# Kernel tuning notes

Measured on AMD Instinct MI355X. Metric: run time of the kernel, lower is better.

The kernel has to match this reference:

```python
import jax, jax.numpy as jnp
import numpy as np

N, E, CIN, H, HEADS, B = 50000, 800000, 16, 64, 3, 64
D0 = HEADS * H            # conv1 out (heads concatenated) = 192
D1 = D0 + CIN             # x1 dim = 208
D2 = 2 * D1               # x2 dim = 416
MLP_IN = 3 * D2           # 1248
MLP_HID = MLP_IN // 2     # 624
EPS = 1e-5


def setup_inputs() -> dict:
    key = jax.random.key(0)
    ks = jax.random.split(key, 24)
    r = lambda k, s, sc=0.05: (jax.random.normal(k, s, dtype=jnp.float32) * sc)
    inp = {
        'x': jax.random.normal(ks[0], (N, CIN), dtype=jnp.float32),
        'edge_index': jax.random.randint(ks[1], (2, E), 0, N, dtype=jnp.int32),
        'edge_attr': jax.random.normal(ks[2], (E, 4), dtype=jnp.float32),
        'batch': jnp.sort(jax.random.randint(ks[3], (N,), 0, B, dtype=jnp.int32)),
        # conv1 (GeneralConv, heads=3, concat): msg/edge/self linears -> D0
        'W_msg1': r(ks[4], (CIN, D0)), 'b_msg1': jnp.zeros((D0,), jnp.float32),
        'W_edge1': r(ks[5], (4, D0)), 'b_edge1': jnp.zeros((D0,), jnp.float32),
        'W_self1': r(ks[6], (CIN, D0)), 'b_self1': jnp.zeros((D0,), jnp.float32),
        'g1': jnp.ones((D0,), jnp.float32), 'be1': jnp.zeros((D0,), jnp.float32),
        # conv2 (GeneralConv, heads=1, in==out -> identity self)
        'W_msg2': r(ks[7], (D1, D1)), 'b_msg2': jnp.zeros((D1,), jnp.float32),
        'W_edge2': r(ks[8], (4, D1)), 'b_edge2': jnp.zeros((D1,), jnp.float32),
        'g2': jnp.ones((D1,), jnp.float32), 'be2': jnp.zeros((D1,), jnp.float32),
        # MLP head
        'W_l1': r(ks[9], (MLP_IN, MLP_HID)), 'b_l1': jnp.zeros((MLP_HID,), jnp.float32),
        'alpha': jnp.asarray(0.25, jnp.float32),  # PReLU default
        'W_l2': r(ks[10], (MLP_HID, 2)), 'b_l2': jnp.zeros((2,), jnp.float32),
    }
    return inp


def _bn(h, g, b):
    m = h.mean(axis=0)
    v = h.var(axis=0)  # biased, like torch BatchNorm training mode
    return (h - m) * jax.lax.rsqrt(v + EPS) * g + b


def reference(x, edge_index, edge_attr, batch,
              W_msg1, b_msg1, W_edge1, b_edge1, W_self1, b_self1, g1, be1,
              W_msg2, b_msg2, W_edge2, b_edge2, g2, be2,
              W_l1, b_l1, alpha, W_l2, b_l2):
    src, dst = edge_index[0], edge_index[1]
    # conv1: gather -> linear msg + edge feature -> scatter-add -> + self linear
    m1 = x[src] @ W_msg1 + b_msg1 + edge_attr @ W_edge1 + b_edge1   # [E, D0]
    h1 = jax.ops.segment_sum(m1, dst, num_segments=N) + (x @ W_self1 + b_self1)
    h1 = _bn(h1, g1, be1)
    x1 = jnp.concatenate([h1, x], axis=1)                           # [N, D1]
    # conv2 (identity self-connection since in==out)
    m2 = x1[src] @ W_msg2 + b_msg2 + edge_attr @ W_edge2 + b_edge2  # [E, D1]
    h2 = jax.ops.segment_sum(m2, dst, num_segments=N) + x1
    h2 = _bn(h2, g2, be2)
    x2 = jnp.concatenate([h2, x1], axis=1)                          # [N, D2]
    # global add / mean / max pooling by graph id
    s = jax.ops.segment_sum(x2, batch, num_segments=B)
    cnt = jax.ops.segment_sum(jnp.ones((x2.shape[0], 1), x2.dtype), batch, num_segments=B)
    mean = s / jnp.maximum(cnt, 1.0)
    mx = jax.ops.segment_max(x2, batch, num_segments=B)
    pooled = jnp.concatenate([s, mx, mean], axis=1)                 # [B, 3*D2]
    # MLP head: Linear -> Dropout(0) -> PReLU -> Linear -> log_softmax
    h = pooled @ W_l1 + b_l1
    h = jnp.where(h >= 0, h, alpha * h)
    logits = h @ W_l2 + b_l2
    return jax.nn.log_softmax(logits, axis=-1)
```

## Files before the change

### kernel.cpp

```cpp
#include <hip/hip_runtime.h>

typedef __attribute__((ext_vector_type(8))) short short8;
typedef __attribute__((ext_vector_type(4))) float f32x4;
typedef unsigned short u16;
typedef unsigned int u32;

__device__ __forceinline__ u16 f2bf(float f) {
  u32 u = __float_as_uint(f);
  u = (u + 0x7fffu + ((u >> 16) & 1u)) >> 16;
  return (u16)u;
}
__device__ __forceinline__ float bf2f(u16 v) { return __uint_as_float((u32)v << 16); }
__device__ __forceinline__ void atomAddF(float* p, float v) { unsafeAtomicAdd(p, v); }
__device__ __forceinline__ void addp(float* v, u32 p) {
  v[0] += bf2f((u16)p);
  v[1] += bf2f((u16)(p >> 16));
}

__global__ void prep_k(const float* __restrict__ Wm1, const float* __restrict__ We1,
                       const float* __restrict__ Ws1, const float* __restrict__ Wm2,
                       const float* __restrict__ Wl1, const float* __restrict__ x,
                       const int* __restrict__ batch, u16* __restrict__ Wp1,
                       u16* __restrict__ Wp2, u16* __restrict__ Wp3,
                       u16* __restrict__ xbf, int* __restrict__ gstart,
                       int* __restrict__ gend, int* __restrict__ deg,
                       float* __restrict__ bns1p, float* __restrict__ bns2p, int N, int E) {
  int tid = blockIdx.x * 256 + threadIdx.x;
  if (tid < 64 * 192) {
    int k = tid / 192, n = tid % 192;
    float v = 0.f;
    if (k < 16) v = Wm1[k * 192 + n];
    else if (k < 20) v = We1[(k - 16) * 192 + n];
    else if (k < 36) v = Ws1[(k - 20) * 192 + n];
    Wp1[((k >> 3) * 192 + n) * 8 + (k & 7)] = f2bf(v);
  }
  if (tid < 224 * 208) {
    int k = tid / 208, n = tid % 208;
    float v = (k < 208) ? Wm2[k * 208 + n] : 0.f;
    Wp2[((k >> 3) * 208 + n) * 8 + (k & 7)] = f2bf(v);
  }
  if (tid < N * 8) {
    float2 p = *(const float2*)(x + (size_t)tid * 2);
    *(u32*)(xbf + (size_t)tid * 2) = (u32)f2bf(p.x) | ((u32)f2bf(p.y) << 16);
  }
  if (tid < N) {
    int b = batch[tid];
    if (tid == 0 || batch[tid - 1] != b) gstart[b] = tid;
    if (tid == N - 1 || batch[tid + 1] != b) gend[b] = tid;
    deg[tid] = 0;
  }
  if (tid < 64 * 384) bns1p[tid] = 0.f;
  if (tid < 64 * 832) bns2p[tid] = 0.f;
  if (tid < 1248 * 624) {
    int k = tid / 624, n = tid % 624;
    Wp3[((size_t)(k >> 3) * 624 + n) * 8 + (k & 7)] = f2bf(Wl1[(size_t)k * 624 + n]);
  }
}

__global__ void count_k(const int* __restrict__ ei, int* __restrict__ deg,
                        int* __restrict__ ord, int E) {
  int e = blockIdx.x * 256 + threadIdx.x;
  if (e >= E) return;
  ord[e] = atomicAdd(&deg[ei[E + e]], 1);
}

__global__ void scanA_k(const int* __restrict__ deg, int* __restrict__ bsum, int N) {
  __shared__ int sh[256];
  int t = threadIdx.x;
  int i = blockIdx.x * 256 + t;
  sh[t] = (i < N) ? deg[i] : 0;
  __syncthreads();
  for (int off = 128; off > 0; off >>= 1) {
    if (t < off) sh[t] += sh[t + off];
    __syncthreads();
  }
  if (t == 0) bsum[blockIdx.x] = sh[0];
}

__global__ void scanC_k(const int* __restrict__ deg, const int* __restrict__ bsum,
                        int* __restrict__ rowptr, int N, int nb) {
  __shared__ int sb2[256];
  __shared__ int sh[256];
  int t = threadIdx.x;
  int bv = (t < nb) ? bsum[t] : 0;
  sb2[t] = bv;
  __syncthreads();
  for (int off = 1; off < 256; off <<= 1) {
    int u = (t >= off) ? sb2[t - off] : 0;
    __syncthreads();
    sb2[t] += u;
    __syncthreads();
  }
  int bpref = (blockIdx.x == 0) ? 0 : sb2[blockIdx.x - 1];
  int i = blockIdx.x * 256 + t;
  int d = (i < N) ? deg[i] : 0;
  sh[t] = d;
  __syncthreads();
  for (int off = 1; off < 256; off <<= 1) {
    int u = (t >= off) ? sh[t - off] : 0;
    __syncthreads();
    sh[t] += u;
    __syncthreads();
  }
  int excl = sh[t] - d + bpref;
  if (i < N) {
    rowptr[i] = excl;
    if (i == N - 1) rowptr[N] = excl + d;
  }
}

__global__ void scatter_k(const int* __restrict__ ei, const float* __restrict__ ea,
                          const int* __restrict__ ord, const int* __restrict__ rowptr,
                          int4* __restrict__ se16, int E) {
  int e = blockIdx.x * 256 + threadIdx.x;
  if (e >= E) return;
  int s = ei[e], d = ei[E + e];
  float4 w = *(const float4*)(ea + (size_t)e * 4);
  int slot = rowptr[d] + ord[e];
  int4 ent;
  ent.x = s;
  ent.y = (int)((u32)f2bf(w.x) | ((u32)f2bf(w.y) << 16));
  ent.z = (int)((u32)f2bf(w.z) | ((u32)f2bf(w.w) << 16));
  ent.w = 0;
  se16[slot] = ent;
}

__global__ void __launch_bounds__(512) conv1_k(
    const int4* __restrict__ se16, const int* __restrict__ rowptr,
    const u16* __restrict__ xbf, const u16* __restrict__ Bp,
    const float* __restrict__ bm1, const float* __restrict__ be1,
    const float* __restrict__ bs1, u16* __restrict__ acc1c, u16* __restrict__ h1bf,
    float* __restrict__ bns1p, int N) {
  __shared__ __align__(16) u16 Uls[32][72];
  __shared__ float degls[32];
  int tid = threadIdx.x;
  int nl = tid >> 4, q = tid & 15;
  int n = blockIdx.x * 32 + nl;
  bool nval = n < N;
  int j0 = nval ? rowptr[n] : 0;
  int j1 = nval ? rowptr[n + 1] : 0;
  float v[20];
#pragma unroll
  for (int i = 0; i < 20; ++i) v[i] = 0.f;
  {
    int j = j0 + q;
    bool a0 = j < j1, a1 = (j + 16) < j1;
    int jj0 = a0 ? j : 0;
    int jj1 = a1 ? (j + 16) : 0;
    int4 p0 = se16[jj0];
    int4 p1 = se16[jj1];
    const uint4* xs0 = (const uint4*)(xbf + (size_t)(a0 ? p0.x : 0) * 16);
    uint4 x00 = xs0[0], x01 = xs0[1];
    const uint4* xs1 = (const uint4*)(xbf + (size_t)(a1 ? p1.x : 0) * 16);
    uint4 x10 = xs1[0], x11 = xs1[1];
    if (a0) {
      addp(v + 0, x00.x); addp(v + 2, x00.y); addp(v + 4, x00.z); addp(v + 6, x00.w);
      addp(v + 8, x01.x); addp(v + 10, x01.y); addp(v + 12, x01.z); addp(v + 14, x01.w);
      addp(v + 16, (u32)p0.y); addp(v + 18, (u32)p0.z);
    }
    if (a1) {
      addp(v + 0, x10.x); addp(v + 2, x10.y); addp(v + 4, x10.z); addp(v + 6, x10.w);
      addp(v + 8, x11.x); addp(v + 10, x11.y); addp(v + 12, x11.z); addp(v + 14, x11.w);
      addp(v + 16, (u32)p1.y); addp(v + 18, (u32)p1.z);
    }
    for (j += 32; j < j1; j += 16) {
      int4 p = se16[j];
      const uint4* xs = (const uint4*)(xbf + (size_t)p.x * 16);
      uint4 x0 = xs[0], x1 = xs[1];
      addp(v + 0, x0.x); addp(v + 2, x0.y); addp(v + 4, x0.z); addp(v + 6, x0.w);
      addp(v + 8, x1.x); addp(v + 10, x1.y); addp(v + 12, x1.z); addp(v + 14, x1.w);
      addp(v + 16, (u32)p.y); addp(v + 18, (u32)p.z);
    }
  }
#pragma unroll
  for (int i = 0; i < 20; ++i) {
    v[i] += __shfl_xor(v[i], 1);
    v[i] += __shfl_xor(v[i], 2);
    v[i] += __shfl_xor(v[i], 4);
    v[i] += __shfl_xor(v[i], 8);
  }
  float degf = (float)(j1 - j0);
  const u16* xr = xbf + (size_t)n * 16;
  {
    u32 w2[2];
#pragma unroll
    for (int jj = 0; jj < 2; ++jj) {
      int t0 = q * 4 + 2 * jj, t1 = t0 + 1;
      u16 b0 = (t0 < 20) ? f2bf(v[t0]) : ((t0 < 36 && nval) ? xr[t0 - 20] : (u16)0);
      u16 b1 = (t1 < 20) ? f2bf(v[t1]) : ((t1 < 36 && nval) ? xr[t1 - 20] : (u16)0);
      w2[jj] = (u32)b0 | ((u32)b1 << 16);
    }
    *(uint2*)&Uls[nl][q * 4] = make_uint2(w2[0], w2[1]);
  }
  if (nval) {
    int t0 = q * 2, t1 = t0 + 1;
    float f0 = (t0 < 20) ? v[t0] : ((t0 == 20) ? degf : 0.f);
    float f1 = (t1 < 20) ? v[t1] : ((t1 == 20) ? degf : 0.f);
    *(u32*)(acc1c + (size_t)n * 32 + q * 2) = (u32)f2bf(f0) | ((u32)f2bf(f1) << 16);
  }
  if (q == 0) degls[nl] = degf;
  __syncthreads();
  int w = tid >> 6, lane = tid & 63, rc = lane & 15, qd = lane >> 4;
  int slice = (blockIdx.x & 63) * 384;
  for (int job = w; job < 24; job += 8) {
    int mt = job / 12, nt = job % 12;
    f32x4 acc = {0.f, 0.f, 0.f, 0.f};
#pragma unroll
    for (int kb = 0; kb < 2; ++kb) {
      short8 av = *(const short8*)&Uls[mt * 16 + rc][kb * 32 + qd * 8];
      short8 bv = *(const short8*)(Bp + (size_t)((kb * 4 + qd) * 192 + nt * 16 + rc) * 8);
      acc = __builtin_amdgcn_mfma_f32_16x16x32_bf16(av, bv, acc, 0, 0, 0);
    }
    int col = nt * 16 + rc;
    float bb = bm1[col] + be1[col], bsv = bs1[col];
    float ps = 0.f, pq = 0.f;
#pragma unroll
    for (int r = 0; r < 4; ++r) {
      int ml = mt * 16 + qd * 4 + r;
      int m = blockIdx.x * 32 + ml;
      float val = acc[r] + degls[ml] * bb + bsv;
      if (m < N) {
        h1bf[(size_t)m * 192 + col] = f2bf(val);
        ps += val;
        pq += val * val;
      }
    }
    ps += __shfl_xor(ps, 16); ps += __shfl_xor(ps, 32);
    pq += __shfl_xor(pq, 16); pq += __shfl_xor(pq, 32);
    if (qd == 0) {
      atomAddF(&bns1p[slice + col], ps);
      atomAddF(&bns1p[slice + 192 + col], pq);
    }
  }
}

__global__ void bnfin1_k(const float* __restrict__ bns1p, const float* __restrict__ g1,
                         const float* __restrict__ bta1, float Ninv,
                         float* __restrict__ aff1) {
  int c = threadIdx.x;
  if (c >= 192) return;
  float sm = 0.f, sq = 0.f;
  for (int k = 0; k < 64; ++k) {
    sm += bns1p[k * 384 + c];
    sq += bns1p[k * 384 + 192 + c];
  }
  float m1 = sm * Ninv;
  float var = sq * Ninv - m1 * m1;
  float s1 = g1[c] * rsqrtf(var + 1e-5f);
  aff1[c] = s1;
  aff1[192 + c] = bta1[c] - m1 * s1;
}

__global__ void __launch_bounds__(512) conv2_k(
    const int4* __restrict__ se16, const int* __restrict__ rowptr,
    const u16* __restrict__ acc1c, const u16* __restrict__ h1bf,
    const u16* __restrict__ xbf, const u16* __restrict__ Bp1, const u16* __restrict__ Bp2,
    const float* __restrict__ bm1, const float* __restrict__ be1,
    const float* __restrict__ bs1, const float* __restrict__ aff1,
    const float* __restrict__ We2, const float* __restrict__ bm2,
    const float* __restrict__ be2, float* __restrict__ bns2p,
    u16* __restrict__ h2bf, int N) {
  __shared__ __align__(16) u16 Uls[32][72];
  __shared__ __align__(16) u16 Vls[32][232];
  __shared__ __align__(16) u16 X1ls[32][208];
  __shared__ float degls[32], sdegls[32], eals[32][4];
  int tid = threadIdx.x;
  int nl = tid >> 4, q = tid & 15;
  int n = blockIdx.x * 32 + nl;
  bool nval = n < N;
  int j0 = nval ? rowptr[n] : 0;
  int j1 = nval ? rowptr[n + 1] : 0;
  int base = blockIdx.x * 32;

  uint4 sg0, sg1, sgx;
  int r0 = tid / 24, c0 = tid % 24;
  int r1 = (tid + 512) / 24, c1 = (tid + 512) % 24;
  {
    int gr = base + r0;
    sg0 = (gr < N) ? *(const uint4*)(h1bf + (size_t)gr * 192 + c0 * 8)
                   : make_uint4(0, 0, 0, 0);
  }
  if (tid < 256) {
    int gr = base + r1;
    sg1 = (gr < N) ? *(const uint4*)(h1bf + (size_t)gr * 192 + c1 * 8)
                   : make_uint4(0, 0, 0, 0);
  }
  if (tid < 64) {
    int gr = base + (tid >> 1);
    sgx = (gr < N) ? *(const uint4*)(xbf + (size_t)gr * 16 + (tid & 1) * 8)
                   : make_uint4(0, 0, 0, 0);
  }

  float v[21];
#pragma unroll
  for (int i = 0; i < 21; ++i) v[i] = 0.f;
  {
    int j = j0 + q;
    bool a0 = j < j1, a1 = (j + 16) < j1;
    int jj0 = a0 ? j : 0;
    int jj1 = a1 ? (j + 16) : 0;
    int4 p0 = se16[jj0];
    int4 p1 = se16[jj1];
    const uint4* cr0 = (const uint4*)(acc1c + (size_t)(a0 ? p0.x : 0) * 32);
    uint4 c00 = cr0[0], c01 = cr0[1], c02 = cr0[2];
    const uint4* cr1 = (const uint4*)(acc1c + (size_t)(a1 ? p1.x : 0) * 32);
    uint4 c10 = cr1[0], c11 = cr1[1], c12 = cr1[2];
    if (a0) {
      addp(v + 0, c00.x); addp(v + 2, c00.y); addp(v + 4, c00.z); addp(v + 6, c00.w);
      addp(v + 8, c01.x); addp(v + 10, c01.y); addp(v + 12, c01.z); addp(v + 14, c01.w);
      addp(v + 16, c02.x); addp(v + 18, c02.y);
      v[20] += bf2f((u16)c02.z);
    }
    if (a1) {
      addp(v + 0, c10.x); addp(v + 2, c10.y); addp(v + 4, c10.z); addp(v + 6, c10.w);
      addp(v + 8, c11.x); addp(v + 10, c11.y); addp(v + 12, c11.z); addp(v + 14, c11.w);
      addp(v + 16, c12.x); addp(v + 18, c12.y);
      v[20] += bf2f((u16)c12.z);
    }
    for (j += 32; j < j1; j += 16) {
      int s = se16[j].x;
      const uint4* cr = (const uint4*)(acc1c + (size_t)s * 32);
      uint4 c0 = cr[0], c1 = cr[1], c2 = cr[2];
      addp(v + 0, c0.x); addp(v + 2, c0.y); addp(v + 4, c0.z); addp(v + 6, c0.w);
      addp(v + 8, c1.x); addp(v + 10, c1.y); addp(v + 12, c1.z); addp(v + 14, c1.w);
      addp(v + 16, c2.x); addp(v + 18, c2.y);
      v[20] += bf2f((u16)c2.z);
    }
  }

  *(uint4*)&X1ls[r0][c0 * 8] = sg0;
  if (tid < 256) *(uint4*)&X1ls[r1][c1 * 8] = sg1;
  if (tid < 64) *(uint4*)&X1ls[tid >> 1][192 + (tid & 1) * 8] = sgx;

#pragma unroll
  for (int i = 0; i < 21; ++i) {
    v[i] += __shfl_xor(v[i], 1);
    v[i] += __shfl_xor(v[i], 2);
    v[i] += __shfl_xor(v[i], 4);
    v[i] += __shfl_xor(v[i], 8);
  }
  const u16* selfr = acc1c + (size_t)n * 32;
  {
    u32 w2[2];
#pragma unroll
    for (int jj = 0; jj < 2; ++jj) {
      int t0 = q * 4 + 2 * jj, t1 = t0 + 1;
      u16 b0 = (t0 < 20) ? f2bf(v[t0]) : ((t0 < 36 && nval) ? selfr[t0 - 20] : (u16)0);
      u16 b1 = (t1 < 20) ? f2bf(v[t1]) : ((t1 < 36 && nval) ? selfr[t1 - 20] : (u16)0);
      w2[jj] = (u32)b0 | ((u32)b1 << 16);
    }
    *(uint2*)&Uls[nl][q * 4] = make_uint2(w2[0], w2[1]);
  }
  {
    int t0 = q * 2, t1 = t0 + 1;
    u16 b0 = (t0 < 16 && nval) ? selfr[t0] : (u16)0;
    u16 b1 = (t1 < 16 && nval) ? selfr[t1] : (u16)0;
    *(u32*)&Vls[nl][192 + q * 2] = (u32)b0 | ((u32)b1 << 16);
  }
  if (q == 0) sdegls[nl] = v[20];
  if (q == 1) degls[nl] = nval ? bf2f(selfr[20]) : 0.f;
  if (q == 2) {
#pragma unroll
    for (int k = 0; k < 4; ++k) eals[nl][k] = nval ? bf2f(selfr[16 + k]) : 0.f;
  }
  __syncthreads();
  int w = tid >> 6, lane = tid & 63, rc = lane & 15, qd = lane >> 4;
  for (int job = w; job < 24; job += 8) {
    int mt = job / 12, nt = job % 12;
    f32x4 acc = {0.f, 0.f, 0.f, 0.f};
#pragma unroll
    for (int kb = 0; kb < 2; ++kb) {
      short8 av = *(const short8*)&Uls[mt * 16 + rc][kb * 32 + qd * 8];
      short8 bv = *(const short8*)(Bp1 + (size_t)((kb * 4 + qd) * 192 + nt * 16 + rc) * 8);
      acc = __builtin_amdgcn_mfma_f32_16x16x32_bf16(av, bv, acc, 0, 0, 0);
    }
    int col = nt * 16 + rc;
    float s1 = aff1[col], t1 = aff1[192 + col];
    float bb = bm1[col] + be1[col], bsv = bs1[col];
#pragma unroll
    for (int r = 0; r < 4; ++r) {
      int ml = mt * 16 + qd * 4 + r;
      float qv = acc[r] + sdegls[ml] * bb + degls[ml] * bsv;
      Vls[ml][col] = f2bf(qv * s1 + degls[ml] * t1);
    }
  }
  __syncthreads();
  int slice = (blockIdx.x & 63) * 832;
  for (int job = w; job < 26; job += 8) {
    int mt = job / 13, nt = job % 13;
    f32x4 acc = {0.f, 0.f, 0.f, 0.f};
#pragma unroll
    for (int kb = 0; kb < 7; ++kb) {
      short8 av = *(const short8*)&Vls[mt * 16 + rc][kb * 32 + qd * 8];
      short8 bv = *(const short8*)(Bp2 + (size_t)((kb * 4 + qd) * 208 + nt * 16 + rc) * 8);
      acc = __builtin_amdgcn_mfma_f32_16x16x32_bf16(av, bv, acc, 0, 0, 0);
    }
    int col = nt * 16 + rc;
    float w0 = We2[col], w1 = We2[208 + col], w2 = We2[416 + col], w3 = We2[624 + col];
    float bb2 = bm2[col] + be2[col];
    bool c192 = col < 192;
    float s1 = c192 ? aff1[col] : 0.f;
    float t1 = c192 ? aff1[192 + col] : 0.f;
    float ps = 0.f, pq = 0.f;
#pragma unroll
    for (int r = 0; r < 4; ++r) {
      int ml = mt * 16 + qd * 4 + r;
      int m = blockIdx.x * 32 + ml;
      bool mv = m < N;
      float x1 = bf2f(X1ls[ml][col]);
      if (c192) x1 = x1 * s1 + t1;
      float val = acc[r] + eals[ml][0] * w0 + eals[ml][1] * w1 + eals[ml][2] * w2 +
                  eals[ml][3] * w3 + degls[ml] * bb2 + x1;
      if (mv) {
        h2bf[(size_t)m * 208 + col] = f2bf(val);
        ps += val;
        pq += val * val;
      }
    }
    ps += __shfl_xor(ps, 16); ps += __shfl_xor(ps, 32);
    pq += __shfl_xor(pq, 16); pq += __shfl_xor(pq, 32);
    if (qd == 0) {
      atomAddF(&bns2p[slice + col], ps);
      atomAddF(&bns2p[slice + 416 + col], pq);
    }
  }
}

__global__ void bnfin2_k(const float* __restrict__ bns2p, const float* __restrict__ aff1,
                         const float* __restrict__ g2, const float* __restrict__ bta2,
                         float Ninv, float* __restrict__ aff) {
  int f = blockIdx.x * 256 + threadIdx.x;
  if (f >= 416) return;
  float sc, sh;
  if (f < 208) {
    float sm = 0.f, sq = 0.f;
    for (int k = 0; k < 64; ++k) {
      sm += bns2p[k * 832 + f];
      sq += bns2p[k * 832 + 416 + f];
    }
    float m2 = sm * Ninv;
    float var = sq * Ninv - m2 * m2;
    sc = g2[f] * rsqrtf(var + 1e-5f);
    sh = bta2[f] - m2 * sc;
  } else if (f < 400) {
    sc = aff1[f - 208];
    sh = aff1[192 + (f - 208)];
  } else {
    sc = 1.f;
    sh = 0.f;
  }
  aff[f] = sc;
  aff[416 + f] = sh;
}

__global__ void pool_k(const u16* __restrict__ h2bf, const u16* __restrict__ h1bf,
                       const u16* __restrict__ xbf, const float* __restrict__ aff,
                       const int* __restrict__ gstart, const int* __restrict__ gend,
                       float* __restrict__ psp, float* __restrict__ pmp) {
  int b = blockIdx.x, sub = blockIdx.y;
  int t = threadIdx.x;
  if (t >= 208) return;
  int s0 = gstart[b], e0 = gend[b];
  int cnt = (s0 <= e0) ? e0 - s0 + 1 : 0;
  int per = (cnt + 15) >> 4;
  int n0 = s0 + sub * per;
  int n1 = min(n0 + per, s0 + cnt);
  int f = 2 * t;
  const u16* src;
  int stride;
  if (f < 208) { src = h2bf + f; stride = 208; }
  else if (f < 400) { src = h1bf + (f - 208); stride = 192; }
  else { src = xbf + (f - 400); stride = 16; }
  float sc0 = aff[f], sc1 = aff[f + 1];
  float sh0 = aff[416 + f], sh1 = aff[417 + f];
  float s0f = 0.f, s1f = 0.f, m0f = -3.4e38f, m1f = -3.4e38f;
  for (int n = n0; n < n1; ++n) {
    u32 p = *(const u32*)(src + (size_t)n * stride);
    float v0 = bf2f((u16)p) * sc0 + sh0;
    float v1 = bf2f((u16)(p >> 16)) * sc1 + sh1;
    s0f += v0; s1f += v1;
    m0f = fmaxf(m0f, v0); m1f = fmaxf(m1f, v1);
  }
  size_t idx = ((size_t)(b * 16 + sub)) * 416 + f;
  *(float2*)(psp + idx) = make_float2(s0f, s1f);
  *(float2*)(pmp + idx) = make_float2(m0f, m1f);
}

__global__ void pooledprep_k(const float* __restrict__ psp, const float* __restrict__ pmp,
                             const int* __restrict__ gstart, const int* __restrict__ gend,
                             u16* __restrict__ Apool) {
  int b = blockIdx.x, t = threadIdx.x;
  int cnt = gend[b] - gstart[b] + 1;
  float inv = 1.f / (float)max(cnt, 1);
  for (int f = t; f < 416; f += 256) {
    float s = 0.f, m = -3.4e38f;
    for (int k = 0; k < 16; ++k) {
      size_t idx = ((size_t)(b * 16 + k)) * 416 + f;
      s += psp[idx];
      m = fmaxf(m, pmp[idx]);
    }
    u16* row = Apool + (size_t)b * 1248;
    row[f] = f2bf(s);
    row[416 + f] = f2bf((cnt > 0) ? m : 0.f);
    row[832 + f] = f2bf(s * inv);
  }
}

__global__ void __launch_bounds__(256) mlpgemm_k(const u16* __restrict__ A,
                                                 const u16* __restrict__ Bp,
                                                 const float* __restrict__ b1,
                                                 const float* __restrict__ al,
                                                 float* __restrict__ hid) {
  __shared__ __align__(16) float part[3][64][4];
  int tid = threadIdx.x;
  int w = tid >> 6, lane = tid & 63;
  int mt = blockIdx.x, nt = blockIdx.y;
  int rc = lane & 15, qd = lane >> 4;
  f32x4 acc = {0.f, 0.f, 0.f, 0.f};
  const u16* Ap = A + (size_t)(mt * 16 + rc) * 1248 + qd * 8;
  const u16* Bq = Bp + (size_t)(qd * 624 + nt * 16 + rc) * 8;
  for (int kb = w; kb < 39; kb += 4) {
    short8 av = *(const short8*)(Ap + kb * 32);
    short8 bv = *(const short8*)(Bq + (size_t)kb * 4 * 624 * 8);
    acc = __builtin_amdgcn_mfma_f32_16x16x32_bf16(av, bv, acc, 0, 0, 0);
  }
  if (w > 0) *(f32x4*)&part[w - 1][lane][0] = acc;
  __syncthreads();
  if (w == 0) {
#pragma unroll
    for (int j = 0; j < 3; ++j) {
      f32x4 p = *(const f32x4*)&part[j][lane][0];
      acc[0] += p[0]; acc[1] += p[1]; acc[2] += p[2]; acc[3] += p[3];
    }
    int col = nt * 16 + rc;
    float bb = b1[col], alpha = al[0];
    int m0 = mt * 16 + qd * 4;
#pragma unroll
    for (int r = 0; r < 4; ++r) {
      float v = acc[r] + bb;
      hid[(size_t)(m0 + r) * 624 + col] = (v >= 0.f) ? v : alpha * v;
    }
  }
}

__global__ void head_k(const float* __restrict__ hid, const float* __restrict__ W2,
                       const float* __restrict__ b2, float* __restrict__ out) {
  int b = blockIdx.x, t = threadIdx.x;
  float p0 = 0.f, p1 = 0.f;
  for (int k = t; k < 624; k += 64) {
    float h = hid[(size_t)b * 624 + k];
    p0 += h * W2[k * 2];
    p1 += h * W2[k * 2 + 1];
  }
#pragma unroll
  for (int off = 32; off > 0; off >>= 1) {
    p0 += __shfl_down(p0, off);
    p1 += __shfl_down(p1, off);
  }
  if (t == 0) {
    float l0 = p0 + b2[0], l1 = p1 + b2[1];
    float m = fmaxf(l0, l1);
    float lse = m + logf(expf(l0 - m) + expf(l1 - m));
    out[b * 2] = l0 - lse;
    out[b * 2 + 1] = l1 - lse;
  }
}

extern "C" void kernel_launch(void* const* d_in, const int* in_sizes, int n_in,
                              void* d_out, int out_size, void* d_ws, size_t ws_size,
                              hipStream_t stream) {
  const float* x = (const float*)d_in[0];
  const int* ei = (const int*)d_in[1];
  const float* ea = (const float*)d_in[2];
  const int* batch = (const int*)d_in[3];
  const float* Wm1 = (const float*)d_in[4];
  const float* bm1 = (const float*)d_in[5];
  const float* We1 = (const float*)d_in[6];
  const float* be1 = (const float*)d_in[7];
  const float* Ws1 = (const float*)d_in[8];
  const float* bs1 = (const float*)d_in[9];
  const float* g1 = (const float*)d_in[10];
  const float* bta1 = (const float*)d_in[11];
  const float* Wm2 = (const float*)d_in[12];
  const float* bm2 = (const float*)d_in[13];
  const float* We2 = (const float*)d_in[14];
  const float* be2 = (const float*)d_in[15];
  const float* g2 = (const float*)d_in[16];
  const float* bta2 = (const float*)d_in[17];
  const float* Wl1 = (const float*)d_in[18];
  const float* bl1 = (const float*)d_in[19];
  const float* alpha = (const float*)d_in[20];
  const float* Wl2 = (const float*)d_in[21];
  const float* bl2 = (const float*)d_in[22];
  float* out = (float*)d_out;

  const int N = in_sizes[3];
  const int E = in_sizes[2] / 4;
  const int nb = (N + 255) / 256;
  const float Ninv = 1.f / (float)N;

  float* ws = (float*)d_ws;
  size_t o = 0;
  u16* acc1c = (u16*)(ws + o); o += (size_t)N * 16;
  u16* h2bf = (u16*)(ws + o);  o += (size_t)N * 104;
  u16* h1bf = (u16*)(ws + o);  o += (size_t)N * 96;
  u16* xbf = (u16*)(ws + o);   o += (size_t)N * 8;
  u16* Wp1 = (u16*)(ws + o);   o += 6144;
  u16* Wp2 = (u16*)(ws + o);   o += 23296;
  u16* Wp3 = (u16*)(ws + o);   o += 389376;
  u16* Apool = (u16*)(ws + o); o += 39936;
  float* hid = ws + o;    o += 64 * 624;
  float* bns1p = ws + o;  o += 64 * 384;
  float* bns2p = ws + o;  o += 64 * 832;
  float* aff1 = ws + o;   o += 384;
  float* aff = ws + o;    o += 832;
  float* psp = ws + o;    o += (size_t)64 * 16 * 416;
  float* pmp = ws + o;    o += (size_t)64 * 16 * 416;
  int* gstart = (int*)(ws + o); o += 64;
  int* gend = (int*)(ws + o);   o += 64;
  int* deg = (int*)(ws + o);    o += N;
  int* rowptr = (int*)(ws + o); o += N + 1;
  int* ord = (int*)(ws + o);    o += E;
  int* bsum = (int*)(ws + o);   o += 256;
  o = (o + 3) & ~(size_t)3;
  int4* se16 = (int4*)(ws + o); o += (size_t)4 * E;

  const int gconv = (N + 31) / 32;
  prep_k<<<(E + 255) / 256, 256, 0, stream>>>(Wm1, We1, Ws1, Wm2, Wl1, x, batch, Wp1, Wp2,
                                              Wp3, xbf, gstart, gend, deg, bns1p, bns2p,
                                              N, E);
  count_k<<<(E + 255) / 256, 256, 0, stream>>>(ei, deg, ord, E);
  scanA_k<<<nb, 256, 0, stream>>>(deg, bsum, N);
  scanC_k<<<nb, 256, 0, stream>>>(deg, bsum, rowptr, N, nb);
  scatter_k<<<(E + 255) / 256, 256, 0, stream>>>(ei, ea, ord, rowptr, se16, E);
  conv1_k<<<gconv, 512, 0, stream>>>(se16, rowptr, xbf, Wp1, bm1, be1, bs1, acc1c, h1bf,
                                     bns1p, N);
  bnfin1_k<<<1, 256, 0, stream>>>(bns1p, g1, bta1, Ninv, aff1);
  conv2_k<<<gconv, 512, 0, stream>>>(se16, rowptr, acc1c, h1bf, xbf, Wp1, Wp2, bm1, be1,
                                     bs1, aff1, We2, bm2, be2, bns2p, h2bf, N);
  bnfin2_k<<<2, 256, 0, stream>>>(bns2p, aff1, g2, bta2, Ninv, aff);
  pool_k<<<dim3(64, 16), 256, 0, stream>>>(h2bf, h1bf, xbf, aff, gstart, gend, psp, pmp);
  pooledprep_k<<<64, 256, 0, stream>>>(psp, pmp, gstart, gend, Apool);
  mlpgemm_k<<<dim3(4, 39), 256, 0, stream>>>(Apool, Wp3, bl1, alpha, hid);
  head_k<<<64, 64, 0, stream>>>(hid, Wl2, bl2, out);
}
```

Baseline: 289.2 us.

## Split fused gather+GEMM conv kernels into separate gather and MFMA kernels

Each conv kernel, which gathered neighbour features and then ran an MFMA GEMM in one launch, is split into a lightweight 256-thread gather kernel (16 nodes per block) and a separate GEMM kernel that reads the compacted aggregates from global memory. The second gather now writes a new bf16 acc2 buffer, which the GEMM kernel reloads. The aim is better occupancy and latency hiding in the irregular gather phase, free of the shared memory and register footprint of the GEMM phase. The cost is two extra launches and an extra global round trip for the aggregated features.

```diff
diff --git a/kernel.cpp b/kernel.cpp
--- a/kernel.cpp
+++ b/kernel.cpp
@@ -125,17 +125,12 @@
   se16[slot] = ent;
 }
 
-__global__ void __launch_bounds__(512) conv1_k(
+__global__ void __launch_bounds__(256) gath1_k(
     const int4* __restrict__ se16, const int* __restrict__ rowptr,
-    const u16* __restrict__ xbf, const u16* __restrict__ Bp,
-    const float* __restrict__ bm1, const float* __restrict__ be1,
-    const float* __restrict__ bs1, u16* __restrict__ acc1c, u16* __restrict__ h1bf,
-    float* __restrict__ bns1p, int N) {
-  __shared__ __align__(16) u16 Uls[32][72];
-  __shared__ float degls[32];
+    const u16* __restrict__ xbf, u16* __restrict__ acc1c, int N) {
   int tid = threadIdx.x;
   int nl = tid >> 4, q = tid & 15;
-  int n = blockIdx.x * 32 + nl;
+  int n = blockIdx.x * 16 + nl;
   bool nval = n < N;
   int j0 = nval ? rowptr[n] : 0;
   int j1 = nval ? rowptr[n + 1] : 0;
@@ -179,118 +174,24 @@
     v[i] += __shfl_xor(v[i], 4);
     v[i] += __shfl_xor(v[i], 8);
   }
-  float degf = (float)(j1 - j0);
-  const u16* xr = xbf + (size_t)n * 16;
-  {
-    u32 w2[2];
-#pragma unroll
-    for (int jj = 0; jj < 2; ++jj) {
-      int t0 = q * 4 + 2 * jj, t1 = t0 + 1;
-      u16 b0 = (t0 < 20) ? f2bf(v[t0]) : ((t0 < 36 && nval) ? xr[t0 - 20] : (u16)0);
-      u16 b1 = (t1 < 20) ? f2bf(v[t1]) : ((t1 < 36 && nval) ? xr[t1 - 20] : (u16)0);
-      w2[jj] = (u32)b0 | ((u32)b1 << 16);
-    }
-    *(uint2*)&Uls[nl][q * 4] = make_uint2(w2[0], w2[1]);
-  }
   if (nval) {
+    float degf = (float)(j1 - j0);
     int t0 = q * 2, t1 = t0 + 1;
     float f0 = (t0 < 20) ? v[t0] : ((t0 == 20) ? degf : 0.f);
     float f1 = (t1 < 20) ? v[t1] : ((t1 == 20) ? degf : 0.f);
     *(u32*)(acc1c + (size_t)n * 32 + q * 2) = (u32)f2bf(f0) | ((u32)f2bf(f1) << 16);
   }
-  if (q == 0) degls[nl] = degf;
-  __syncthreads();
-  int w = tid >> 6, lane = tid & 63, rc = lane & 15, qd = lane >> 4;
-  int slice = (blockIdx.x & 63) * 384;
-  for (int job = w; job < 24; job += 8) {
-    int mt = job / 12, nt = job % 12;
-    f32x4 acc = {0.f, 0.f, 0.f, 0.f};
-#pragma unroll
-    for (int kb = 0; kb < 2; ++kb) {
-      short8 av = *(const short8*)&Uls[mt * 16 + rc][kb * 32 + qd * 8];
-      short8 bv = *(const short8*)(Bp + (size_t)((kb * 4 + qd) * 192 + nt * 16 + rc) * 8);
-      acc = __builtin_amdgcn_mfma_f32_16x16x32_bf16(av, bv, acc, 0, 0, 0);
-    }
-    int col = nt * 16 + rc;
-    float bb = bm1[col] + be1[col], bsv = bs1[col];
-    float ps = 0.f, pq = 0.f;
-#pragma unroll
-    for (int r = 0; r < 4; ++r) {
-      int ml = mt * 16 + qd * 4 + r;
-      int m = blockIdx.x * 32 + ml;
-      float val = acc[r] + degls[ml] * bb + bsv;
-      if (m < N) {
-        h1bf[(size_t)m * 192 + col] = f2bf(val);
-        ps += val;
-        pq += val * val;
-      }
-    }
-    ps += __shfl_xor(ps, 16); ps += __shfl_xor(ps, 32);
-    pq += __shfl_xor(pq, 16); pq += __shfl_xor(pq, 32);
-    if (qd == 0) {
-      atomAddF(&bns1p[slice + col], ps);
-      atomAddF(&bns1p[slice + 192 + col], pq);
-    }
-  }
-}
-
-__global__ void bnfin1_k(const float* __restrict__ bns1p, const float* __restrict__ g1,
-                         const float* __restrict__ bta1, float Ninv,
-                         float* __restrict__ aff1) {
-  int c = threadIdx.x;
-  if (c >= 192) return;
-  float sm = 0.f, sq = 0.f;
-  for (int k = 0; k < 64; ++k) {
-    sm += bns1p[k * 384 + c];
-    sq += bns1p[k * 384 + 192 + c];
-  }
-  float m1 = sm * Ninv;
-  float var = sq * Ninv - m1 * m1;
-  float s1 = g1[c] * rsqrtf(var + 1e-5f);
-  aff1[c] = s1;
-  aff1[192 + c] = bta1[c] - m1 * s1;
-}
-
-__global__ void __launch_bounds__(512) conv2_k(
+}
+
+__global__ void __launch_bounds__(256) gath2_k(
     const int4* __restrict__ se16, const int* __restrict__ rowptr,
-    const u16* __restrict__ acc1c, const u16* __restrict__ h1bf,
-    const u16* __restrict__ xbf, const u16* __restrict__ Bp1, const u16* __restrict__ Bp2,
-    const float* __restrict__ bm1, const float* __restrict__ be1,
-    const float* __restrict__ bs1, const float* __restrict__ aff1,
-    const float* __restrict__ We2, const float* __restrict__ bm2,
-    const float* __restrict__ be2, float* __restrict__ bns2p,
-    u16* __restrict__ h2bf, int N) {
-  __shared__ __align__(16) u16 Uls[32][72];
-  __shared__ __align__(16) u16 Vls[32][232];
-  __shared__ __align__(16) u16 X1ls[32][208];
-  __shared__ float degls[32], sdegls[32], eals[32][4];
+    const u16* __restrict__ acc1c, u16* __restrict__ acc2, int N) {
   int tid = threadIdx.x;
   int nl = tid >> 4, q = tid & 15;
-  int n = blockIdx.x * 32 + nl;
+  int n = blockIdx.x * 16 + nl;
   bool nval = n < N;
   int j0 = nval ? rowptr[n] : 0;
   int j1 = nval ? rowptr[n + 1] : 0;
-  int base = blockIdx.x * 32;
-
-  uint4 sg0, sg1, sgx;
-  int r0 = tid / 24, c0 = tid % 24;
-  int r1 = (tid + 512) / 24, c1 = (tid + 512) % 24;
-  {
-    int gr = base + r0;
-    sg0 = (gr < N) ? *(const uint4*)(h1bf + (size_t)gr * 192 + c0 * 8)
-                   : make_uint4(0, 0, 0, 0);
-  }
-  if (tid < 256) {
-    int gr = base + r1;
-    sg1 = (gr < N) ? *(const uint4*)(h1bf + (size_t)gr * 192 + c1 * 8)
-                   : make_uint4(0, 0, 0, 0);
-  }
-  if (tid < 64) {
-    int gr = base + (tid >> 1);
-    sgx = (gr < N) ? *(const uint4*)(xbf + (size_t)gr * 16 + (tid & 1) * 8)
-                   : make_uint4(0, 0, 0, 0);
-  }
-
   float v[21];
 #pragma unroll
   for (int i = 0; i < 21; ++i) v[i] = 0.f;
@@ -327,11 +228,6 @@
       v[20] += bf2f((u16)c2.z);
     }
   }
-
-  *(uint4*)&X1ls[r0][c0 * 8] = sg0;
-  if (tid < 256) *(uint4*)&X1ls[r1][c1 * 8] = sg1;
-  if (tid < 64) *(uint4*)&X1ls[tid >> 1][192 + (tid & 1) * 8] = sgx;
-
 #pragma unroll
   for (int i = 0; i < 21; ++i) {
     v[i] += __shfl_xor(v[i], 1);
@@ -339,29 +235,155 @@
     v[i] += __shfl_xor(v[i], 4);
     v[i] += __shfl_xor(v[i], 8);
   }
-  const u16* selfr = acc1c + (size_t)n * 32;
+  if (nval && q < 12) {
+    int t0 = q * 2, t1 = t0 + 1;
+    float f0 = (t0 < 20) ? v[t0] : ((t0 == 20) ? v[20] : 0.f);
+    float f1 = (t1 < 20) ? v[t1] : ((t1 == 20) ? v[20] : 0.f);
+    *(u32*)(acc2 + (size_t)n * 24 + q * 2) = (u32)f2bf(f0) | ((u32)f2bf(f1) << 16);
+  }
+}
+
+__global__ void __launch_bounds__(512) mm1_k(
+    const u16* __restrict__ acc1c, const u16* __restrict__ xbf,
+    const u16* __restrict__ Bp, const float* __restrict__ bm1,
+    const float* __restrict__ be1, const float* __restrict__ bs1,
+    u16* __restrict__ h1bf, float* __restrict__ bns1p, int N) {
+  __shared__ __align__(16) u16 Uls[32][72];
+  __shared__ float degls[32];
+  int tid = threadIdx.x;
+  int nl = tid >> 4, q = tid & 15;
+  int n = blockIdx.x * 32 + nl;
+  bool nval = n < N;
+  u32 w0 = 0, w1 = 0;
+  if (nval) {
+    if (q < 5) {
+      w0 = *(const u32*)(acc1c + (size_t)n * 32 + q * 4);
+      w1 = *(const u32*)(acc1c + (size_t)n * 32 + q * 4 + 2);
+    } else if (q < 9) {
+      int o = q * 4 - 20;
+      w0 = *(const u32*)(xbf + (size_t)n * 16 + o);
+      w1 = *(const u32*)(xbf + (size_t)n * 16 + o + 2);
+    }
+  }
+  *(uint2*)&Uls[nl][q * 4] = make_uint2(w0, w1);
+  if (q == 0) degls[nl] = nval ? bf2f(acc1c[(size_t)n * 32 + 20]) : 0.f;
+  __syncthreads();
+  int w = tid >> 6, lane = tid & 63, rc = lane & 15, qd = lane >> 4;
+  int slice = (blockIdx.x & 63) * 384;
+  for (int job = w; job < 24; job += 8) {
+    int mt = job / 12, nt = job % 12;
+    f32x4 acc = {0.f, 0.f, 0.f, 0.f};
+#pragma unroll
+    for (int kb = 0; kb < 2; ++kb) {
+      short8 av = *(const short8*)&Uls[mt * 16 + rc][kb * 32 + qd * 8];
+      short8 bv = *(const short8*)(Bp + (size_t)((kb * 4 + qd) * 192 + nt * 16 + rc) * 8);
+      acc = __builtin_amdgcn_mfma_f32_16x16x32_bf16(av, bv, acc, 0, 0, 0);
+    }
+    int col = nt * 16 + rc;
+    float bb = bm1[col] + be1[col], bsv = bs1[col];
+    float ps = 0.f, pq = 0.f;
+#pragma unroll
+    for (int r = 0; r < 4; ++r) {
+      int ml = mt * 16 + qd * 4 + r;
+      int m = blockIdx.x * 32 + ml;
+      float val = acc[r] + degls[ml] * bb + bsv;
+      if (m < N) {
+        h1bf[(size_t)m * 192 + col] = f2bf(val);
+        ps += val;
+        pq += val * val;
+      }
+    }
+    ps += __shfl_xor(ps, 16); ps += __shfl_xor(ps, 32);
+    pq += __shfl_xor(pq, 16); pq += __shfl_xor(pq, 32);
+    if (qd == 0) {
+      atomAddF(&bns1p[slice + col], ps);
+      atomAddF(&bns1p[slice + 192 + col], pq);
+    }
+  }
+}
+
+__global__ void bnfin1_k(const float* __restrict__ bns1p, const float* __restrict__ g1,
+                         const float* __restrict__ bta1, float Ninv,
+                         float* __restrict__ aff1) {
+  int c = threadIdx.x;
+  if (c >= 192) return;
+  float sm = 0.f, sq = 0.f;
+  for (int k = 0; k < 64; ++k) {
+    sm += bns1p[k * 384 + c];
+    sq += bns1p[k * 384 + 192 + c];
+  }
+  float m1 = sm * Ninv;
+  float var = sq * Ninv - m1 * m1;
+  float s1 = g1[c] * rsqrtf(var + 1e-5f);
+  aff1[c] = s1;
+  aff1[192 + c] = bta1[c] - m1 * s1;
+}
+
+__global__ void __launch_bounds__(512) mm2_k(
+    const u16* __restrict__ acc1c, const u16* __restrict__ acc2,
+    const u16* __restrict__ h1bf, const u16* __restrict__ xbf,
+    const u16* __restrict__ Bp1, const u16* __restrict__ Bp2,
+    const float* __restrict__ bm1, const float* __restrict__ be1,
+    const float* __restrict__ bs1, const float* __restrict__ aff1,
+    const float* __restrict__ We2, const float* __restrict__ bm2,
+    const float* __restrict__ be2, float* __restrict__ bns2p,
+    u16* __restrict__ h2bf, int N) {
+  __shared__ __align__(16) u16 Uls[32][72];
+  __shared__ __align__(16) u16 Vls[32][232];
+  __shared__ __align__(16) u16 X1ls[32][208];
+  __shared__ float degls[32], sdegls[32], eals[32][4];
+  int tid = threadIdx.x;
+  int nl = tid >> 4, q = tid & 15;
+  int n = blockIdx.x * 32 + nl;
+  bool nval = n < N;
+  int base = blockIdx.x * 32;
+
   {
-    u32 w2[2];
-#pragma unroll
-    for (int jj = 0; jj < 2; ++jj) {
-      int t0 = q * 4 + 2 * jj, t1 = t0 + 1;
-      u16 b0 = (t0 < 20) ? f2bf(v[t0]) : ((t0 < 36 && nval) ? selfr[t0 - 20] : (u16)0);
-      u16 b1 = (t1 < 20) ? f2bf(v[t1]) : ((t1 < 36 && nval) ? selfr[t1 - 20] : (u16)0);
-      w2[jj] = (u32)b0 | ((u32)b1 << 16);
-    }
-    *(uint2*)&Uls[nl][q * 4] = make_uint2(w2[0], w2[1]);
-  }
+    int r0 = tid / 24, c0 = tid % 24;
+    int gr = base + r0;
+    uint4 sg = (gr < N) ? *(const uint4*)(h1bf + (size_t)gr * 192 + c0 * 8)
+                        : make_uint4(0, 0, 0, 0);
+    *(uint4*)&X1ls[r0][c0 * 8] = sg;
+  }
+  if (tid < 256) {
+    int r1 = (tid + 512) / 24, c1 = (tid + 512) % 24;
+    int gr = base + r1;
+    uint4 sg = (gr < N) ? *(const uint4*)(h1bf + (size_t)gr * 192 + c1 * 8)
+                        : make_uint4(0, 0, 0, 0);
+    *(uint4*)&X1ls[r1][c1 * 8] = sg;
+  }
+  if (tid < 64) {
+    int gr = base + (tid >> 1);
+    uint4 sg = (gr < N) ? *(const uint4*)(xbf + (size_t)gr * 16 + (tid & 1) * 8)
+                        : make_uint4(0, 0, 0, 0);
+    *(uint4*)&X1ls[tid >> 1][192 + (tid & 1) * 8] = sg;
+  }
+
   {
-    int t0 = q * 2, t1 = t0 + 1;
-    u16 b0 = (t0 < 16 && nval) ? selfr[t0] : (u16)0;
-    u16 b1 = (t1 < 16 && nval) ? selfr[t1] : (u16)0;
-    *(u32*)&Vls[nl][192 + q * 2] = (u32)b0 | ((u32)b1 << 16);
-  }
-  if (q == 0) sdegls[nl] = v[20];
-  if (q == 1) degls[nl] = nval ? bf2f(selfr[20]) : 0.f;
+    u32 w0 = 0, w1 = 0;
+    if (nval) {
+      if (q < 5) {
+        w0 = *(const u32*)(acc2 + (size_t)n * 24 + q * 4);
+        w1 = *(const u32*)(acc2 + (size_t)n * 24 + q * 4 + 2);
+      } else if (q < 9) {
+        int o = q * 4 - 20;
+        w0 = *(const u32*)(acc1c + (size_t)n * 32 + o);
+        w1 = *(const u32*)(acc1c + (size_t)n * 32 + o + 2);
+      }
+    }
+    *(uint2*)&Uls[nl][q * 4] = make_uint2(w0, w1);
+  }
+  {
+    u32 w = 0;
+    if (nval && q < 8) w = *(const u32*)(acc1c + (size_t)n * 32 + q * 2);
+    *(u32*)&Vls[nl][192 + q * 2] = w;
+  }
+  if (q == 0) sdegls[nl] = nval ? bf2f(acc2[(size_t)n * 24 + 20]) : 0.f;
+  if (q == 1) degls[nl] = nval ? bf2f(acc1c[(size_t)n * 32 + 20]) : 0.f;
   if (q == 2) {
 #pragma unroll
-    for (int k = 0; k < 4; ++k) eals[nl][k] = nval ? bf2f(selfr[16 + k]) : 0.f;
+    for (int k = 0; k < 4; ++k)
+      eals[nl][k] = nval ? bf2f(acc1c[(size_t)n * 32 + 16 + k]) : 0.f;
   }
   __syncthreads();
   int w = tid >> 6, lane = tid & 63, rc = lane & 15, qd = lane >> 4;
@@ -602,6 +624,7 @@
   float* ws = (float*)d_ws;
   size_t o = 0;
   u16* acc1c = (u16*)(ws + o); o += (size_t)N * 16;
+  u16* acc2 = (u16*)(ws + o);  o += (size_t)N * 12;
   u16* h2bf = (u16*)(ws + o);  o += (size_t)N * 104;
   u16* h1bf = (u16*)(ws + o);  o += (size_t)N * 96;
   u16* xbf = (u16*)(ws + o);   o += (size_t)N * 8;
@@ -625,7 +648,8 @@
   o = (o + 3) & ~(size_t)3;
   int4* se16 = (int4*)(ws + o); o += (size_t)4 * E;
 
-  const int gconv = (N + 31) / 32;
+  const int ggath = (N + 15) / 16;
+  const int gmm = (N + 31) / 32;
   prep_k<<<(E + 255) / 256, 256, 0, stream>>>(Wm1, We1, Ws1, Wm2, Wl1, x, batch, Wp1, Wp2,
                                               Wp3, xbf, gstart, gend, deg, bns1p, bns2p,
                                               N, E);
@@ -633,11 +657,12 @@
   scanA_k<<<nb, 256, 0, stream>>>(deg, bsum, N);
   scanC_k<<<nb, 256, 0, stream>>>(deg, bsum, rowptr, N, nb);
   scatter_k<<<(E + 255) / 256, 256, 0, stream>>>(ei, ea, ord, rowptr, se16, E);
-  conv1_k<<<gconv, 512, 0, stream>>>(se16, rowptr, xbf, Wp1, bm1, be1, bs1, acc1c, h1bf,
-                                     bns1p, N);
+  gath1_k<<<ggath, 256, 0, stream>>>(se16, rowptr, xbf, acc1c, N);
+  mm1_k<<<gmm, 512, 0, stream>>>(acc1c, xbf, Wp1, bm1, be1, bs1, h1bf, bns1p, N);
   bnfin1_k<<<1, 256, 0, stream>>>(bns1p, g1, bta1, Ninv, aff1);
-  conv2_k<<<gconv, 512, 0, stream>>>(se16, rowptr, acc1c, h1bf, xbf, Wp1, Wp2, bm1, be1,
-                                     bs1, aff1, We2, bm2, be2, bns2p, h2bf, N);
+  gath2_k<<<ggath, 256, 0, stream>>>(se16, rowptr, acc1c, acc2, N);
+  mm2_k<<<gmm, 512, 0, stream>>>(acc1c, acc2, h1bf, xbf, Wp1, Wp2, bm1, be1, bs1, aff1,
+                                 We2, bm2, be2, bns2p, h2bf, N);
   bnfin2_k<<<2, 256, 0, stream>>>(bns2p, aff1, g2, bta2, Ninv, aff);
   pool_k<<<dim3(64, 16), 256, 0, stream>>>(h2bf, h1bf, xbf, aff, gstart, gend, psp, pmp);
   pooledprep_k<<<64, 256, 0, stream>>>(psp, pmp, gstart, gend, Apool);
```

Result: no change. 292.7 us (+1.2%).
